# Kernel tuning notes

Hardware: AMD Instinct MI355X
Metric: run time of the kernel (lower is better)

## Reference

```python
import jax, jax.numpy as jnp
import numpy as np

N_POINTS = 8192
N_QUERIES = 8192
MAX_NEIGHBORS = 128  # pad cap; expected ~34 neighbors at radius 0.1 in unit cube


def setup_inputs() -> dict:
    key = jax.random.key(0)
    kp, kq = jax.random.split(key)
    points = jax.random.uniform(kp, (N_POINTS, 3), dtype=jnp.float32)
    queries = jax.random.uniform(kq, (N_QUERIES, 3), dtype=jnp.float32)
    radius = jnp.float32(0.1)
    return {"points": points, "queries": queries, "radius": radius}


def reference(points, queries, radius):
    """Fixed-radius neighbor search, metric=L2 (squared distances), no query-point
    exclusion. Returns padded neighbor indices [Q,K] (-1 = padding), exact
    neighbors_row_splits [Q+1], and padded squared distances [Q,K]."""
    K = MAX_NEIGHBORS
    N = points.shape[0]
    # squared L2 pairwise distances via |q|^2 + |p|^2 - 2 q.p  -> [Q, N]
    p2 = jnp.sum(points * points, axis=-1)          # [N]
    q2 = jnp.sum(queries * queries, axis=-1)        # [Q]
    d2 = q2[:, None] + p2[None, :] - 2.0 * (queries @ points.T)
    d2 = jnp.maximum(d2, 0.0)
    # L2 metric: neighbor iff dist <= radius, i.e. dist^2 <= radius^2
    mask = d2 <= radius * radius                    # [Q, N]
    counts = jnp.sum(mask, axis=1).astype(jnp.int32)
    # exclusive prefix sum with total as last element -> [Q+1]
    neighbors_row_splits = jnp.concatenate(
        [jnp.zeros((1,), jnp.int32), jnp.cumsum(counts)])
    # first K neighbor indices per query, in ascending index order
    key_idx = jnp.where(mask, jnp.arange(N, dtype=jnp.int32), N)  # N = sentinel
    neg_topk, _ = jax.lax.top_k(-key_idx, K)        # K smallest keys
    idx = -neg_topk                                  # [Q, K], sentinel = N
    valid = idx < N
    safe_idx = jnp.clip(idx, 0, N - 1)
    dist = jnp.take_along_axis(d2, safe_idx, axis=1)  # [Q, K]
    neighbors_index = jnp.where(valid, idx, -1)
    neighbors_distance = jnp.where(valid, dist, 0.0)
    return neighbors_index, neighbors_row_splits, neighbors_distance
```

## Files before the change

### kernel.cpp

```cpp
#include <hip/hip_runtime.h>
#include <hip/hip_bf16.h>

#define NPTS 8192
#define NQRY 8192
#define KMAX 128
#define TILE 2048

__global__ __launch_bounds__(256) void frs_main_kernel(
    const float* __restrict__ pts, const float* __restrict__ qrs,
    const float* __restrict__ rad,
    float* __restrict__ out_idx, float* __restrict__ out_dist,
    int* __restrict__ counts) {
  __shared__ float4 sp[TILE];

  const int lane = threadIdx.x & 63;
  const int wid = threadIdx.x >> 6;
  const int q = blockIdx.x * 4 + wid;

  const float q0 = qrs[q * 3 + 0];
  const float q1 = qrs[q * 3 + 1];
  const float q2 = qrs[q * 3 + 2];
  const float r = rad[0];
  const float r2 = __fmul_rn(r, r);
  const float qq = __fadd_rn(
      __fadd_rn(__fmul_rn(q0, q0), __fmul_rn(q1, q1)), __fmul_rn(q2, q2));

  const unsigned long long lanemask_lt = (1ull << lane) - 1ull;
  int count = 0;

  float* const oi = out_idx + (size_t)q * KMAX;
  float* const od = out_dist + (size_t)q * KMAX;

  for (int t0 = 0; t0 < NPTS; t0 += TILE) {
    __syncthreads();
    for (int i = threadIdx.x; i < TILE; i += 256) {
      const int pi = t0 + i;
      const float x = pts[pi * 3 + 0];
      const float y = pts[pi * 3 + 1];
      const float z = pts[pi * 3 + 2];
      const float pp = __fadd_rn(
          __fadd_rn(__fmul_rn(x, x), __fmul_rn(y, y)), __fmul_rn(z, z));
      sp[i] = make_float4(x, y, z, pp);
    }
    __syncthreads();

    for (int j = lane; j < TILE; j += 64) {
      const float4 p = sp[j];
      const float dot = __fadd_rn(
          __fadd_rn(__fmul_rn(q0, p.x), __fmul_rn(q1, p.y)),
          __fmul_rn(q2, p.z));
      float d2 = __fsub_rn(__fadd_rn(qq, p.w), __fmul_rn(2.0f, dot));
      d2 = fmaxf(d2, 0.0f);
      const bool hit = d2 <= r2;
      const unsigned long long m = __ballot(hit);
      if (hit) {
        const int pos = count + __popcll(m & lanemask_lt);
        if (pos < KMAX) {
          oi[pos] = (float)(t0 + j);
          od[pos] = d2;
        }
      }
      count += __popcll(m);
    }
  }

  for (int s = count + lane; s < KMAX; s += 64) {
    oi[s] = -1.0f;
    od[s] = 0.0f;
  }
  if (lane == 0) counts[q] = count;
}

__global__ __launch_bounds__(1024) void frs_scan_kernel(
    const int* __restrict__ counts, float* __restrict__ row_splits) {
  const int t = threadIdx.x;
  const int base = t * 8;
  int c[8];
  int s = 0;
#pragma unroll
  for (int i = 0; i < 8; i++) {
    c[i] = counts[base + i];
    s += c[i];
  }
  const int lane = t & 63;
  const int wid = t >> 6;
  int incl = s;
#pragma unroll
  for (int off = 1; off < 64; off <<= 1) {
    const int v = __shfl_up(incl, off, 64);
    if (lane >= off) incl += v;
  }
  __shared__ int wpart[16];
  if (lane == 63) wpart[wid] = incl;
  __syncthreads();
  if (t == 0) {
    int run = 0;
    for (int i = 0; i < 16; i++) {
      const int v = wpart[i];
      wpart[i] = run;
      run += v;
    }
  }
  __syncthreads();
  const int excl = wpart[wid] + (incl - s);
  int run = excl;
#pragma unroll
  for (int i = 0; i < 8; i++) {
    row_splits[base + i] = (float)run;
    run += c[i];
  }
  if (t == 1023) row_splits[NQRY] = (float)run;
}

extern "C" void kernel_launch(void* const* d_in, const int* in_sizes, int n_in,
                              void* d_out, int out_size, void* d_ws, size_t ws_size,
                              hipStream_t stream) {
  const float* pts = (const float*)d_in[0];
  const float* qrs = (const float*)d_in[1];
  const float* rad = (const float*)d_in[2];

  float* out = (float*)d_out;
  float* out_idx = out;
  float* row_splits = out + (size_t)NQRY * KMAX;
  float* out_dist = row_splits + (NQRY + 1);

  int* counts = (int*)d_ws;

  frs_main_kernel<<<NQRY / 4, 256, 0, stream>>>(pts, qrs, rad, out_idx,
                                                out_dist, counts);
  frs_scan_kernel<<<1, 1024, 0, stream>>>(counts, row_splits);
}
```

Baseline: 103.3 us.

## Add uniform grid spatial hashing for radius search with brute-force verification pass

Builds a 10x10x10 cell grid by counting-sorting points in a single block, then each query wave scans only neighboring cells and rank-sorts its hits by original index. A follow-up kernel recomputes the full brute-force result to verify and repair each query's output. This aims to cut distance work to nearby cells, but the verification kernel repeats the full O(QN) scan and adds extra launches.

Result: slower. 159.7 us (+54.6%).

```diff
diff --git a/kernel.cpp b/kernel.cpp
--- a/kernel.cpp
+++ b/kernel.cpp
@@ -4,14 +4,285 @@
 #define NPTS 8192
 #define NQRY 8192
 #define KMAX 128
-#define TILE 2048
-
-__global__ __launch_bounds__(256) void frs_main_kernel(
-    const float* __restrict__ pts, const float* __restrict__ qrs,
-    const float* __restrict__ rad,
+#define G 10
+#define NCELL 1000
+#define RANGE_EPS 1e-5f
+
+#define WS_COUNTS 0
+#define WS_SORTED 32768
+#define WS_CSTART 163840
+#define WS_NEED 167872
+
+__device__ __forceinline__ int cell_clamp(float v) {
+  int c = (int)floorf(v * 10.0f);
+  return c < 0 ? 0 : (c > G - 1 ? G - 1 : c);
+}
+
+__global__ __launch_bounds__(1024) void frs_build(
+    const float* __restrict__ pts, float4* __restrict__ sorted,
+    int* __restrict__ cell_start) {
+  __shared__ int s_cnt[NCELL];
+  __shared__ int s_tmp[16];
+  const int t = threadIdx.x;
+  if (t < NCELL) s_cnt[t] = 0;
+  __syncthreads();
+
+  float px[8], py[8], pz[8];
+  int pc[8];
+#pragma unroll
+  for (int k = 0; k < 8; ++k) {
+    const int pid = k * 1024 + t;
+    px[k] = pts[pid * 3 + 0];
+    py[k] = pts[pid * 3 + 1];
+    pz[k] = pts[pid * 3 + 2];
+    pc[k] = (cell_clamp(px[k]) * G + cell_clamp(py[k])) * G + cell_clamp(pz[k]);
+    atomicAdd(&s_cnt[pc[k]], 1);
+  }
+  __syncthreads();
+
+  const int lane = t & 63, wid = t >> 6;
+  const int v = (t < NCELL) ? s_cnt[t] : 0;
+  int incl = v;
+#pragma unroll
+  for (int off = 1; off < 64; off <<= 1) {
+    const int u = __shfl_up(incl, off, 64);
+    if (lane >= off) incl += u;
+  }
+  if (lane == 63) s_tmp[wid] = incl;
+  __syncthreads();
+  if (t == 0) {
+    int run = 0;
+    for (int i = 0; i < 16; ++i) {
+      const int x = s_tmp[i];
+      s_tmp[i] = run;
+      run += x;
+    }
+  }
+  __syncthreads();
+  const int excl = s_tmp[wid] + (incl - v);
+  if (t < NCELL) {
+    cell_start[t] = excl;
+    s_cnt[t] = excl;
+  }
+  if (t == NCELL - 1) cell_start[NCELL] = excl + v;
+  __syncthreads();
+
+#pragma unroll
+  for (int k = 0; k < 8; ++k) {
+    const int pos = atomicAdd(&s_cnt[pc[k]], 1);
+    sorted[pos] = make_float4(px[k], py[k], pz[k], __int_as_float(k * 1024 + t));
+  }
+}
+
+__global__ __launch_bounds__(256) void frs_query_g(
+    const float4* __restrict__ sorted, const int* __restrict__ cstart,
+    const float* __restrict__ qrs, const float* __restrict__ rad,
     float* __restrict__ out_idx, float* __restrict__ out_dist,
     int* __restrict__ counts) {
-  __shared__ float4 sp[TILE];
+  __shared__ int hidx[4][KMAX];
+  __shared__ float hd2[4][KMAX];
+
+  const int lane = threadIdx.x & 63;
+  const int wid = threadIdx.x >> 6;
+  const int q = blockIdx.x * 4 + wid;
+
+  const float qx = qrs[q * 3 + 0];
+  const float qy = qrs[q * 3 + 1];
+  const float qz = qrs[q * 3 + 2];
+  const float r = rad[0];
+  const float r2 = __fmul_rn(r, r);
+  const float qq = __fadd_rn(
+      __fadd_rn(__fmul_rn(qx, qx), __fmul_rn(qy, qy)), __fmul_rn(qz, qz));
+
+  const float rm = r + RANGE_EPS;
+  const int x0 = cell_clamp(qx - rm), x1 = cell_clamp(qx + rm);
+  const int y0 = cell_clamp(qy - rm), y1 = cell_clamp(qy + rm);
+  const int z0 = cell_clamp(qz - rm), z1 = cell_clamp(qz + rm);
+
+  const unsigned long long lt = (1ull << lane) - 1ull;
+  int cnt = 0;
+
+  for (int cx = x0; cx <= x1; ++cx) {
+    for (int cy = y0; cy <= y1; ++cy) {
+      const int rb = (cx * G + cy) * G;
+      const int s = cstart[rb + z0];
+      const int e = cstart[rb + z1 + 1];
+      for (int jb = s; jb < e; jb += 64) {
+        const int j = jb + lane;
+        const bool act = j < e;
+        const float4 p = sorted[act ? j : s];
+        const float pp = __fadd_rn(
+            __fadd_rn(__fmul_rn(p.x, p.x), __fmul_rn(p.y, p.y)),
+            __fmul_rn(p.z, p.z));
+        const float dot = __fadd_rn(
+            __fadd_rn(__fmul_rn(qx, p.x), __fmul_rn(qy, p.y)),
+            __fmul_rn(qz, p.z));
+        float d2 = __fsub_rn(__fadd_rn(qq, pp), __fmul_rn(2.0f, dot));
+        d2 = fmaxf(d2, 0.0f);
+        const bool hit = act && (d2 <= r2);
+        const unsigned long long m = __ballot(hit);
+        if (hit) {
+          const int pos = cnt + __popcll(m & lt);
+          if (pos < KMAX) {
+            hidx[wid][pos] = __float_as_int(p.w);
+            hd2[wid][pos] = d2;
+          }
+        }
+        cnt += __popcll(m);
+      }
+    }
+  }
+
+  const int cc = cnt < KMAX ? cnt : KMAX;
+  float* const oi = out_idx + (size_t)q * KMAX;
+  float* const od = out_dist + (size_t)q * KMAX;
+
+  const int i0 = lane, i1 = lane + 64;
+  const int k0 = (i0 < cc) ? hidx[wid][i0] : 0;
+  const float v0 = (i0 < cc) ? hd2[wid][i0] : 0.0f;
+  const int k1 = (i1 < cc) ? hidx[wid][i1] : 0;
+  const float v1 = (i1 < cc) ? hd2[wid][i1] : 0.0f;
+  int r0 = 0, r1 = 0;
+  for (int s = 0; s < cc; ++s) {
+    const int ks = hidx[wid][s];
+    r0 += (ks < k0);
+    r1 += (ks < k1);
+  }
+  if (i0 < cc) {
+    oi[r0] = (float)k0;
+    od[r0] = v0;
+  } else {
+    oi[i0] = -1.0f;
+    od[i0] = 0.0f;
+  }
+  if (i1 < cc) {
+    oi[r1] = (float)k1;
+    od[r1] = v1;
+  } else {
+    oi[i1] = -1.0f;
+    od[i1] = 0.0f;
+  }
+  if (lane == 0) counts[q] = cnt;
+}
+
+__global__ __launch_bounds__(512) void frs_check(
+    const float* __restrict__ pts, const float* __restrict__ qrs,
+    const float* __restrict__ rad, float* __restrict__ out_idx,
+    float* __restrict__ out_dist, int* __restrict__ counts) {
+  __shared__ float4 sp[2048];
+  __shared__ int s_flag;
+
+  const int lane = threadIdx.x & 63;
+  const int wid = threadIdx.x >> 6;
+  const int q = blockIdx.x * 8 + wid;
+  if (threadIdx.x == 0) s_flag = 0;
+
+  const float qx = qrs[q * 3 + 0];
+  const float qy = qrs[q * 3 + 1];
+  const float qz = qrs[q * 3 + 2];
+  const float r = rad[0];
+  const float r2 = __fmul_rn(r, r);
+  const float qq = __fadd_rn(
+      __fadd_rn(__fmul_rn(qx, qx), __fmul_rn(qy, qy)), __fmul_rn(qz, qz));
+
+  const unsigned long long lt = (1ull << lane) - 1ull;
+  float* const oi = out_idx + (size_t)q * KMAX;
+  float* const od = out_dist + (size_t)q * KMAX;
+
+  int cnt = 0;
+  bool ok = true;
+
+  for (int t0 = 0; t0 < NPTS; t0 += 2048) {
+    __syncthreads();
+    for (int i = threadIdx.x; i < 2048; i += 512) {
+      const int pi = t0 + i;
+      const float x = pts[pi * 3 + 0];
+      const float y = pts[pi * 3 + 1];
+      const float z = pts[pi * 3 + 2];
+      const float pp = __fadd_rn(
+          __fadd_rn(__fmul_rn(x, x), __fmul_rn(y, y)), __fmul_rn(z, z));
+      sp[i] = make_float4(x, y, z, pp);
+    }
+    __syncthreads();
+
+    for (int j = lane; j < 2048; j += 64) {
+      const float4 p = sp[j];
+      const float dot = __fadd_rn(
+          __fadd_rn(__fmul_rn(qx, p.x), __fmul_rn(qy, p.y)),
+          __fmul_rn(qz, p.z));
+      float d2 = __fsub_rn(__fadd_rn(qq, p.w), __fmul_rn(2.0f, dot));
+      d2 = fmaxf(d2, 0.0f);
+      const bool hit = d2 <= r2;
+      const unsigned long long m = __ballot(hit);
+      if (hit) {
+        const int pos = cnt + __popcll(m & lt);
+        if (pos < KMAX) {
+          ok = ok && (oi[pos] == (float)(t0 + j)) && (od[pos] == d2);
+        }
+      }
+      cnt += __popcll(m);
+    }
+  }
+  const int cc = cnt < KMAX ? cnt : KMAX;
+  for (int s = cc + lane; s < KMAX; s += 64) {
+    ok = ok && (oi[s] == -1.0f) && (od[s] == 0.0f);
+  }
+  ok = ok && (counts[q] == cnt);
+
+  const bool repair = !__all(ok);
+  if (lane == 0 && repair) atomicOr(&s_flag, 1);
+  __syncthreads();
+
+  if (s_flag) {
+    int rcnt = 0;
+    for (int t0 = 0; t0 < NPTS; t0 += 2048) {
+      __syncthreads();
+      for (int i = threadIdx.x; i < 2048; i += 512) {
+        const int pi = t0 + i;
+        const float x = pts[pi * 3 + 0];
+        const float y = pts[pi * 3 + 1];
+        const float z = pts[pi * 3 + 2];
+        const float pp = __fadd_rn(
+            __fadd_rn(__fmul_rn(x, x), __fmul_rn(y, y)), __fmul_rn(z, z));
+        sp[i] = make_float4(x, y, z, pp);
+      }
+      __syncthreads();
+      if (repair) {
+        for (int j = lane; j < 2048; j += 64) {
+          const float4 p = sp[j];
+          const float dot = __fadd_rn(
+              __fadd_rn(__fmul_rn(qx, p.x), __fmul_rn(qy, p.y)),
+              __fmul_rn(qz, p.z));
+          float d2 = __fsub_rn(__fadd_rn(qq, p.w), __fmul_rn(2.0f, dot));
+          d2 = fmaxf(d2, 0.0f);
+          const bool hit = d2 <= r2;
+          const unsigned long long m = __ballot(hit);
+          if (hit) {
+            const int pos = rcnt + __popcll(m & lt);
+            if (pos < KMAX) {
+              oi[pos] = (float)(t0 + j);
+              od[pos] = d2;
+            }
+          }
+          rcnt += __popcll(m);
+        }
+      }
+    }
+    if (repair) {
+      for (int s = rcnt + lane; s < KMAX; s += 64) {
+        oi[s] = -1.0f;
+        od[s] = 0.0f;
+      }
+      if (lane == 0) counts[q] = rcnt;
+    }
+  }
+}
+
+__global__ __launch_bounds__(256) void frs_brute(
+    const float* __restrict__ pts, const float* __restrict__ qrs,
+    const float* __restrict__ rad, float* __restrict__ out_idx,
+    float* __restrict__ out_dist, int* __restrict__ counts) {
+  __shared__ float4 sp[2048];
 
   const int lane = threadIdx.x & 63;
   const int wid = threadIdx.x >> 6;
@@ -25,15 +296,15 @@
   const float qq = __fadd_rn(
       __fadd_rn(__fmul_rn(q0, q0), __fmul_rn(q1, q1)), __fmul_rn(q2, q2));
 
-  const unsigned long long lanemask_lt = (1ull << lane) - 1ull;
+  const unsigned long long lt = (1ull << lane) - 1ull;
   int count = 0;
 
   float* const oi = out_idx + (size_t)q * KMAX;
   float* const od = out_dist + (size_t)q * KMAX;
 
-  for (int t0 = 0; t0 < NPTS; t0 += TILE) {
+  for (int t0 = 0; t0 < NPTS; t0 += 2048) {
     __syncthreads();
-    for (int i = threadIdx.x; i < TILE; i += 256) {
+    for (int i = threadIdx.x; i < 2048; i += 256) {
       const int pi = t0 + i;
       const float x = pts[pi * 3 + 0];
       const float y = pts[pi * 3 + 1];
@@ -44,7 +315,7 @@
     }
     __syncthreads();
 
-    for (int j = lane; j < TILE; j += 64) {
+    for (int j = lane; j < 2048; j += 64) {
       const float4 p = sp[j];
       const float dot = __fadd_rn(
           __fadd_rn(__fmul_rn(q0, p.x), __fmul_rn(q1, p.y)),
@@ -54,7 +325,7 @@
       const bool hit = d2 <= r2;
       const unsigned long long m = __ballot(hit);
       if (hit) {
-        const int pos = count + __popcll(m & lanemask_lt);
+        const int pos = count + __popcll(m & lt);
         if (pos < KMAX) {
           oi[pos] = (float)(t0 + j);
           od[pos] = d2;
@@ -124,9 +395,20 @@
   float* row_splits = out + (size_t)NQRY * KMAX;
   float* out_dist = row_splits + (NQRY + 1);
 
-  int* counts = (int*)d_ws;
-
-  frs_main_kernel<<<NQRY / 4, 256, 0, stream>>>(pts, qrs, rad, out_idx,
-                                                out_dist, counts);
+  char* ws = (char*)d_ws;
+  int* counts = (int*)(ws + WS_COUNTS);
+  float4* sorted = (float4*)(ws + WS_SORTED);
+  int* cell_start = (int*)(ws + WS_CSTART);
+
+  if (ws_size >= (size_t)WS_NEED) {
+    frs_build<<<1, 1024, 0, stream>>>(pts, sorted, cell_start);
+    frs_query_g<<<NQRY / 4, 256, 0, stream>>>(sorted, cell_start, qrs, rad,
+                                              out_idx, out_dist, counts);
+    frs_check<<<NQRY / 8, 512, 0, stream>>>(pts, qrs, rad, out_idx, out_dist,
+                                            counts);
+  } else {
+    frs_brute<<<NQRY / 4, 256, 0, stream>>>(pts, qrs, rad, out_idx, out_dist,
+                                            counts);
+  }
   frs_scan_kernel<<<1, 1024, 0, stream>>>(counts, row_splits);
 }
```
